# Kernel tuning notes

Hardware: AMD Instinct MI355X
Metric: run time of the kernel (lower is better)

The kernel has to match this reference:

```python
import jax, jax.numpy as jnp
import numpy as np

B, MAXN, NVT, NINP, NHID, NHEAD, NL, NZ = 1024, 32, 16, 256, 512, 8, 6, 64
HID = MAXN * NHID
EPS = 1e-5
SCALE = 1.0 / np.sqrt(NHID // NHEAD)


def setup_inputs() -> dict:
    key = jax.random.key(0)
    ks = jax.random.split(key, 16)
    s = 0.02
    d = {}
    d["node_types"] = jax.random.randint(ks[0], (B, MAXN), 0, NVT, dtype=jnp.int32)
    d["adj_bits"] = jax.random.randint(ks[1], (B, MAXN, MAXN), 0, 2, dtype=jnp.int32)
    d["Wpos"] = jax.random.normal(ks[2], (MAXN, NINP), jnp.float32) * s
    d["bpos"] = jnp.zeros((NINP,), jnp.float32)
    d["Wnode"] = jax.random.normal(ks[3], (NVT, NINP), jnp.float32) * s
    d["bnode"] = jnp.zeros((NINP,), jnp.float32)
    for i, n in enumerate(["Wq", "Wk", "Wv", "Wo", "W1", "W2"]):
        d["enc_" + n] = jax.random.normal(ks[4 + i], (NL, NHID, NHID), jnp.float32) * s
    for n in ["bq", "bk", "bv", "bo", "b1", "b2"]:
        d["enc_" + n] = jnp.zeros((NL, NHID), jnp.float32)
    d["ln1_g"] = jnp.ones((NL, NHID), jnp.float32)
    d["ln1_b"] = jnp.zeros((NL, NHID), jnp.float32)
    d["ln2_g"] = jnp.ones((NL, NHID), jnp.float32)
    d["ln2_b"] = jnp.zeros((NL, NHID), jnp.float32)
    d["Wfc1"] = jax.random.normal(ks[10], (HID, NZ), jnp.float32) * s
    d["bfc1"] = jnp.zeros((NZ,), jnp.float32)
    d["Wfc2"] = jax.random.normal(ks[11], (HID, NZ), jnp.float32) * s
    d["bfc2"] = jnp.zeros((NZ,), jnp.float32)
    return d


def _ln(x, g, b):
    m = x.mean(-1, keepdims=True)
    v = ((x - m) ** 2).mean(-1, keepdims=True)
    return (x - m) * jax.lax.rsqrt(v + EPS) * g + b


def _dag_attn_bias(adj_bits):
    # _mask_generate: transitive closure via matmul powers; log-depth squaring
    # over a boolean semiring (min(.,1) after each add) gives identical reachability.
    iu = jnp.triu(jnp.ones((MAXN, MAXN), jnp.float32), 1)  # enforce DAG
    adj = adj_bits.astype(jnp.float32) * iu  # [B,N,N]
    reach = adj
    for _ in range(int(np.ceil(np.log2(MAXN)))):
        reach = jnp.minimum(reach + jnp.matmul(reach, reach), 1.0)
    # original: mask = (sum_powers + I) < 0.5 (True=disallowed), then transpose(1,2)
    allowed = (jnp.swapaxes(reach, 1, 2) + jnp.eye(MAXN, dtype=jnp.float32)) > 0.5
    return jnp.where(allowed, 0.0, -jnp.inf)[:, None, :, :]  # [B,1,N,N]


def _encode(node_types, adj_bits, Wpos, bpos, Wnode, bnode,
            enc_Wq, enc_bq, enc_Wk, enc_bk, enc_Wv, enc_bv, enc_Wo, enc_bo,
            ln1_g, ln1_b, enc_W1, enc_b1, enc_W2, enc_b2, ln2_g, ln2_b,
            Wfc1, bfc1, Wfc2, bfc2):
    node_feat = jax.nn.relu(Wnode[node_types] + bnode)               # [B,N,ninp]
    pos_feat = jnp.broadcast_to(Wpos + bpos, (B, MAXN, NINP))        # position = node index
    x = jnp.concatenate([node_feat, pos_feat], -1)                   # [B,N,512]
    bias = _dag_attn_bias(adj_bits)
    dh = NHID // NHEAD
    for l in range(NL):
        q = (x @ enc_Wq[l] + enc_bq[l]).reshape(B, MAXN, NHEAD, dh)
        k = (x @ enc_Wk[l] + enc_bk[l]).reshape(B, MAXN, NHEAD, dh)
        v = (x @ enc_Wv[l] + enc_bv[l]).reshape(B, MAXN, NHEAD, dh)
        s = jnp.einsum('bqhd,bkhd->bhqk', q, k) * SCALE + bias
        a = jax.nn.softmax(s, axis=-1)
        o = jnp.einsum('bhqk,bkhd->bqhd', a, v).reshape(B, MAXN, NHID)
        x = _ln(x + o @ enc_Wo[l] + enc_bo[l], ln1_g[l], ln1_b[l])    # post-LN
        f = jax.nn.relu(x @ enc_W1[l] + enc_b1[l]) @ enc_W2[l] + enc_b2[l]
        x = _ln(x + f, ln2_g[l], ln2_b[l])
    mem = x.reshape(B, HID)
    return mem @ Wfc1 + bfc1, mem @ Wfc2 + bfc2


def reference(node_types, adj_bits, Wpos, bpos, Wnode, bnode,
              enc_Wq, enc_bq, enc_Wk, enc_bk, enc_Wv, enc_bv, enc_Wo, enc_bo,
              ln1_g, ln1_b, enc_W1, enc_b1, enc_W2, enc_b2, ln2_g, ln2_b,
              Wfc1, bfc1, Wfc2, bfc2):
    return _encode(node_types, adj_bits, Wpos, bpos, Wnode, bnode,
                   enc_Wq, enc_bq, enc_Wk, enc_bk, enc_Wv, enc_bv, enc_Wo, enc_bo,
                   ln1_g, ln1_b, enc_W1, enc_b1, enc_W2, enc_b2, ln2_g, ln2_b,
                   Wfc1, bfc1, Wfc2, bfc2)
```

## Files before the change

### kernel.cpp

```cpp
#include <hip/hip_runtime.h>


typedef unsigned short u16;
typedef unsigned int u32;
typedef __attribute__((ext_vector_type(8))) short bf16x8;
typedef __attribute__((ext_vector_type(4))) float f32x4;

#define NB 1024
#define MAXN 32
#define NHID 512
#define NHEAD 8
#define NLAY 6
#define MTOT (NB * MAXN)
#define ATT_SCALE 0.125f
#define LN_EPS 1e-5f

__device__ __forceinline__ float bf2f(u16 h) { return __uint_as_float(((u32)h) << 16); }
__device__ __forceinline__ u16 f2bf(float f) {
  u32 u = __float_as_uint(f);
  return (u16)((u + 0x7fffu + ((u >> 16) & 1u)) >> 16);
}

__device__ __forceinline__ void gload16(const void* g, void* l) {
  __builtin_amdgcn_global_load_lds((const __attribute__((address_space(1))) void*)g,
                                   (__attribute__((address_space(3))) void*)l, 16, 0, 0);
}

__global__ __launch_bounds__(256) void mask_k(const int* __restrict__ adj, u32* __restrict__ mask) {
  __shared__ u32 r[8][32];
  int tid = threadIdx.x;
  int g = tid >> 5, i = tid & 31;
  int b = blockIdx.x * 8 + g;
  const int* ab = adj + ((long)b * 32 + i) * 32;
  u32 m = 0;
  for (int j = i + 1; j < 32; ++j)
    if (ab[j]) m |= (1u << j);
  r[g][i] = m;
  __syncthreads();
  for (int it = 0; it < 5; ++it) {
    u32 cur = r[g][i];
    u32 acc = cur;
    #pragma unroll
    for (int j = 0; j < 32; ++j)
      if ((cur >> j) & 1u) acc |= r[g][j];
    __syncthreads();
    r[g][i] = acc;
    __syncthreads();
  }
  u32 am = 1u << i;
  #pragma unroll
  for (int k = 0; k < 32; ++k) am |= ((r[g][k] >> i) & 1u) << k;
  mask[b * 32 + i] = am;
}

__global__ __launch_bounds__(256) void embed_k(const int* __restrict__ types,
    const float* __restrict__ Wpos, const float* __restrict__ bpos,
    const float* __restrict__ Wnode, const float* __restrict__ bnode,
    float* __restrict__ x, u16* __restrict__ xb) {
  int i = blockIdx.x * 256 + threadIdx.x;
  int row = i >> 7, c = (i & 127) * 4;
  int b = row >> 5, n = row & 31;
  float v[4];
  if (c < 256) {
    int tp = types[b * 32 + n];
    const float* w = &Wnode[tp * 256 + c];
    #pragma unroll
    for (int j = 0; j < 4; ++j) v[j] = fmaxf(w[j] + bnode[c + j], 0.f);
  } else {
    int cc = c - 256;
    const float* w = &Wpos[n * 256 + cc];
    #pragma unroll
    for (int j = 0; j < 4; ++j) v[j] = w[j] + bpos[cc + j];
  }
  long o = (long)row * NHID + c;
  *(float4*)&x[o] = make_float4(v[0], v[1], v[2], v[3]);
  ushort4 h; h.x = f2bf(v[0]); h.y = f2bf(v[1]); h.z = f2bf(v[2]); h.w = f2bf(v[3]);
  *(ushort4*)&xb[o] = h;
}

__global__ __launch_bounds__(256) void tconv_k(const float* __restrict__ W,
    u16* __restrict__ Wt, int n_off, int n_total) {
  __shared__ float tile[32][33];
  int l = blockIdx.z;
  int k0 = blockIdx.x * 32, n0 = blockIdx.y * 32;
  int tx = threadIdx.x & 31, ty = threadIdx.x >> 5;
  const float* src = W + (size_t)l * NHID * NHID;
  #pragma unroll
  for (int i = 0; i < 4; ++i)
    tile[ty + 8 * i][tx] = src[(size_t)(k0 + ty + 8 * i) * NHID + n0 + tx];
  __syncthreads();
  u16* dst = Wt + (size_t)l * n_total * NHID;
  #pragma unroll
  for (int i = 0; i < 4; ++i)
    dst[(size_t)(n_off + n0 + ty + 8 * i) * NHID + k0 + tx] = f2bf(tile[tx][ty + 8 * i]);
}

template <int EPI>
__global__ __launch_bounds__(256, 2) void gemm_bt(
    const u16* __restrict__ A, const u16* __restrict__ Bt,
    const float* __restrict__ bias0, const float* __restrict__ bias1,
    const float* __restrict__ bias2, u16* __restrict__ Cout, int N, int K) {
  __shared__ u16 As[128 * 32];
  __shared__ u16 Bs[128 * 32];
  const int tid = threadIdx.x;
  const int wave = tid >> 6, lane = tid & 63;
  const long m0 = (long)blockIdx.y * 128;
  const int n0 = blockIdx.x * 128;
  const int wr = wave >> 1, wc = wave & 1;
  const int srow = lane >> 2;
  const int skof = (lane & 3) * 8;
  const int fr = lane & 15;
  const int kq = lane >> 4;
  f32x4 acc[4][4] = {};

  for (int k0 = 0; k0 < K; k0 += 32) {
    #pragma unroll
    for (int i = 0; i < 2; ++i) {
      int c = 2 * wave + i;
      gload16(A + (m0 + 16 * c + srow) * (long)K + k0 + skof, &As[c * 512]);
      gload16(Bt + (long)(n0 + 16 * c + srow) * K + k0 + skof, &Bs[c * 512]);
    }
    __syncthreads();
    bf16x8 af[4], bfr[4];
    #pragma unroll
    for (int mi = 0; mi < 4; ++mi)
      af[mi] = *(const bf16x8*)&As[(wr * 64 + mi * 16 + fr) * 32 + kq * 8];
    #pragma unroll
    for (int ni = 0; ni < 4; ++ni)
      bfr[ni] = *(const bf16x8*)&Bs[(wc * 64 + ni * 16 + fr) * 32 + kq * 8];
    #pragma unroll
    for (int mi = 0; mi < 4; ++mi)
      #pragma unroll
      for (int ni = 0; ni < 4; ++ni)
        acc[mi][ni] = __builtin_amdgcn_mfma_f32_16x16x32_bf16(af[mi], bfr[ni], acc[mi][ni], 0, 0, 0);
    __syncthreads();
  }

  #pragma unroll
  for (int ni = 0; ni < 4; ++ni) {
    int n = n0 + wc * 64 + ni * 16 + fr;
    const float* bp = (n < 512) ? bias0 : ((n < 1024) ? bias1 : bias2);
    float bias = bp[n & 511];
    #pragma unroll
    for (int mi = 0; mi < 4; ++mi) {
      long r = m0 + wr * 64 + mi * 16 + kq * 4;
      #pragma unroll
      for (int j = 0; j < 4; ++j) {
        float v = acc[mi][ni][j] + bias;
        if (EPI == 2) v = fmaxf(v, 0.f);
        Cout[(r + j) * (long)N + n] = f2bf(v);
      }
    }
  }
}

__global__ __launch_bounds__(256) void attn_k(const u16* __restrict__ qkv,
    const u32* __restrict__ mask, u16* __restrict__ o) {
  __shared__ u16 p_lds[4][32][40];
  int tid = threadIdx.x;
  int w = tid >> 6, lane = tid & 63;
  int idx = blockIdx.x * 4 + w;
  int b = idx >> 3, h = idx & 7;
  const u16* base = qkv + (long)b * 32 * 1536;
  int g = lane >> 4, r = lane & 15;

  f32x4 s[2][2] = {};
  #pragma unroll
  for (int ks = 0; ks < 2; ++ks) {
    bf16x8 kf[2], qf[2];
    #pragma unroll
    for (int mi = 0; mi < 2; ++mi)
      kf[mi] = *(const bf16x8*)(base + (long)(mi * 16 + r) * 1536 + 512 + h * 64 + ks * 32 + g * 8);
    #pragma unroll
    for (int nj = 0; nj < 2; ++nj)
      qf[nj] = *(const bf16x8*)(base + (long)(nj * 16 + r) * 1536 + h * 64 + ks * 32 + g * 8);
    #pragma unroll
    for (int mi = 0; mi < 2; ++mi)
      #pragma unroll
      for (int nj = 0; nj < 2; ++nj)
        s[mi][nj] = __builtin_amdgcn_mfma_f32_16x16x32_bf16(kf[mi], qf[nj], s[mi][nj], 0, 0, 0);
  }

  #pragma unroll
  for (int nj = 0; nj < 2; ++nj) {
    int q = nj * 16 + r;
    u32 mk = mask[b * 32 + q];
    float v[8];
    float mx = -1e30f;
    #pragma unroll
    for (int mi = 0; mi < 2; ++mi)
      #pragma unroll
      for (int j = 0; j < 4; ++j) {
        int k = mi * 16 + g * 4 + j;
        float val = ((mk >> k) & 1u) ? s[mi][nj][j] * ATT_SCALE : -1e30f;
        v[mi * 4 + j] = val;
        mx = fmaxf(mx, val);
      }
    mx = fmaxf(mx, __shfl_xor(mx, 16));
    mx = fmaxf(mx, __shfl_xor(mx, 32));
    float sum = 0.f;
    #pragma unroll
    for (int i = 0; i < 8; ++i) { v[i] = __expf(v[i] - mx); sum += v[i]; }
    sum += __shfl_xor(sum, 16);
    sum += __shfl_xor(sum, 32);
    float inv = 1.f / sum;
    #pragma unroll
    for (int mi = 0; mi < 2; ++mi) {
      ushort4 pk;
      pk.x = f2bf(v[mi * 4 + 0] * inv);
      pk.y = f2bf(v[mi * 4 + 1] * inv);
      pk.z = f2bf(v[mi * 4 + 2] * inv);
      pk.w = f2bf(v[mi * 4 + 3] * inv);
      *(ushort4*)&p_lds[w][q][mi * 16 + g * 4] = pk;
    }
  }
  __syncthreads();

  bf16x8 pa[2];
  #pragma unroll
  for (int mi = 0; mi < 2; ++mi)
    pa[mi] = *(const bf16x8*)&p_lds[w][mi * 16 + r][g * 8];
  f32x4 oacc[2][4] = {};
  #pragma unroll
  for (int nd = 0; nd < 4; ++nd) {
    bf16x8 vf;
    #pragma unroll
    for (int t = 0; t < 8; ++t)
      vf[t] = *(const short*)(base + (long)(g * 8 + t) * 1536 + 1024 + h * 64 + nd * 16 + r);
    #pragma unroll
    for (int mi = 0; mi < 2; ++mi)
      oacc[mi][nd] = __builtin_amdgcn_mfma_f32_16x16x32_bf16(pa[mi], vf, oacc[mi][nd], 0, 0, 0);
  }
  #pragma unroll
  for (int mi = 0; mi < 2; ++mi)
    #pragma unroll
    for (int j = 0; j < 4; ++j) {
      int q = mi * 16 + g * 4 + j;
      u16* og = o + ((long)b * 32 + q) * NHID + h * 64;
      #pragma unroll
      for (int nd = 0; nd < 4; ++nd)
        og[nd * 16 + r] = f2bf(oacc[mi][nd][j]);
    }
}

__global__ __launch_bounds__(256) void ln_k(float* xio, const u16* __restrict__ t,
    const float* __restrict__ g, const float* __restrict__ b, u16* __restrict__ xb) {
  __shared__ float ps[4], psq[4];
  int tid = threadIdx.x;
  int half = tid >> 7, lt = tid & 127;
  long row = (long)blockIdx.x * 2 + half;
  int c = lt * 4;
  long o = row * NHID + c;
  float4 xv = *(const float4*)&xio[o];
  ushort4 tv = *(const ushort4*)&t[o];
  float y[4] = {xv.x + bf2f(tv.x), xv.y + bf2f(tv.y), xv.z + bf2f(tv.z), xv.w + bf2f(tv.w)};
  float s = y[0] + y[1] + y[2] + y[3];
  float sq = y[0] * y[0] + y[1] * y[1] + y[2] * y[2] + y[3] * y[3];
  #pragma unroll
  for (int off = 32; off; off >>= 1) {
    s += __shfl_down(s, off);
    sq += __shfl_down(sq, off);
  }
  int wave = tid >> 6;
  if ((tid & 63) == 0) { ps[wave] = s; psq[wave] = sq; }
  __syncthreads();
  int w0 = half * 2;
  float S = ps[w0] + ps[w0 + 1], SQ = psq[w0] + psq[w0 + 1];
  float mean = S * (1.f / 512.f);
  float var = SQ * (1.f / 512.f) - mean * mean;
  float inv = rsqrtf(var + LN_EPS);
  float out[4];
  #pragma unroll
  for (int j = 0; j < 4; ++j) out[j] = (y[j] - mean) * inv * g[c + j] + b[c + j];
  *(float4*)&xio[o] = make_float4(out[0], out[1], out[2], out[3]);
  ushort4 hv; hv.x = f2bf(out[0]); hv.y = f2bf(out[1]); hv.z = f2bf(out[2]); hv.w = f2bf(out[3]);
  *(ushort4*)&xb[o] = hv;
}

__global__ __launch_bounds__(256) void fcT_k(const float* __restrict__ W1,
    const float* __restrict__ W2, u16* __restrict__ Wt) {
  __shared__ float t[64][65];
  int sel = blockIdx.y;
  const float* W = sel ? W2 : W1;
  int k0 = blockIdx.x * 64;
  int tx = threadIdx.x & 63, ty = threadIdx.x >> 6;
  #pragma unroll
  for (int i = 0; i < 16; ++i)
    t[ty + 4 * i][tx] = W[(long)(k0 + ty + 4 * i) * 64 + tx];
  __syncthreads();
  #pragma unroll
  for (int i = 0; i < 16; ++i)
    Wt[(long)(sel * 64 + ty + 4 * i) * 16384 + k0 + tx] = f2bf(t[tx][ty + 4 * i]);
}

__global__ __launch_bounds__(256, 2) void gemm_fc(const u16* __restrict__ A,
    const u16* __restrict__ Bt, float* __restrict__ part) {
  __shared__ u16 As[128 * 32];
  __shared__ u16 Bs[128 * 32];
  const int tid = threadIdx.x;
  const int wave = tid >> 6, lane = tid & 63;
  const int ks = blockIdx.x;
  const long m0 = (long)blockIdx.y * 128;
  const int kbase = ks * 512;
  const int wr = wave >> 1, wc = wave & 1;
  const int srow = lane >> 2;
  const int skof = (lane & 3) * 8;
  const int fr = lane & 15;
  const int kq = lane >> 4;
  f32x4 acc[4][4] = {};
  for (int k0 = 0; k0 < 512; k0 += 32) {
    #pragma unroll
    for (int i = 0; i < 2; ++i) {
      int c = 2 * wave + i;
      gload16(A + (m0 + 16 * c + srow) * 16384L + kbase + k0 + skof, &As[c * 512]);
      gload16(Bt + (long)(16 * c + srow) * 16384L + kbase + k0 + skof, &Bs[c * 512]);
    }
    __syncthreads();
    bf16x8 af[4], bfr[4];
    #pragma unroll
    for (int mi = 0; mi < 4; ++mi)
      af[mi] = *(const bf16x8*)&As[(wr * 64 + mi * 16 + fr) * 32 + kq * 8];
    #pragma unroll
    for (int ni = 0; ni < 4; ++ni)
      bfr[ni] = *(const bf16x8*)&Bs[(wc * 64 + ni * 16 + fr) * 32 + kq * 8];
    #pragma unroll
    for (int mi = 0; mi < 4; ++mi)
      #pragma unroll
      for (int ni = 0; ni < 4; ++ni)
        acc[mi][ni] = __builtin_amdgcn_mfma_f32_16x16x32_bf16(af[mi], bfr[ni], acc[mi][ni], 0, 0, 0);
    __syncthreads();
  }
  #pragma unroll
  for (int ni = 0; ni < 4; ++ni) {
    int n = wc * 64 + ni * 16 + fr;
    #pragma unroll
    for (int mi = 0; mi < 4; ++mi) {
      long rr = m0 + wr * 64 + mi * 16 + kq * 4;
      #pragma unroll
      for (int j = 0; j < 4; ++j)
        part[((long)ks * 1024 + rr + j) * 128 + n] = acc[mi][ni][j];
    }
  }
}

__global__ __launch_bounds__(256) void fc_red_k(const float* __restrict__ part,
    const float* __restrict__ bfc1, const float* __restrict__ bfc2,
    float* __restrict__ out) {
  int idx = blockIdx.x * 256 + threadIdx.x;
  int sel = idx >> 16;
  int rem = idx & 65535;
  int b = rem >> 6, z = rem & 63;
  float v = sel ? bfc2[z] : bfc1[z];
  #pragma unroll
  for (int ks = 0; ks < 32; ++ks)
    v += part[((long)ks * 1024 + b) * 128 + sel * 64 + z];
  out[idx] = v;
}

extern "C" void kernel_launch(void* const* d_in, const int* in_sizes, int n_in,
                              void* d_out, int out_size, void* d_ws, size_t ws_size,
                              hipStream_t stream) {
  const int* node_types = (const int*)d_in[0];
  const int* adj_bits = (const int*)d_in[1];
  const float* Wpos = (const float*)d_in[2];
  const float* bpos = (const float*)d_in[3];
  const float* Wnode = (const float*)d_in[4];
  const float* bnode = (const float*)d_in[5];
  const float* eWq = (const float*)d_in[6];
  const float* eWk = (const float*)d_in[7];
  const float* eWv = (const float*)d_in[8];
  const float* eWo = (const float*)d_in[9];
  const float* eW1 = (const float*)d_in[10];
  const float* eW2 = (const float*)d_in[11];
  const float* ebq = (const float*)d_in[12];
  const float* ebk = (const float*)d_in[13];
  const float* ebv = (const float*)d_in[14];
  const float* ebo = (const float*)d_in[15];
  const float* eb1 = (const float*)d_in[16];
  const float* eb2 = (const float*)d_in[17];
  const float* ln1g = (const float*)d_in[18];
  const float* ln1b = (const float*)d_in[19];
  const float* ln2g = (const float*)d_in[20];
  const float* ln2b = (const float*)d_in[21];
  const float* Wfc1 = (const float*)d_in[22];
  const float* bfc1 = (const float*)d_in[23];
  const float* Wfc2 = (const float*)d_in[24];
  const float* bfc2 = (const float*)d_in[25];

  char* ws = (char*)d_ws;
  size_t off = 0;
  auto carve = [&](size_t bytes) {
    void* p = ws + off;
    off += (bytes + 255) & ~(size_t)255;
    return p;
  };
  u16* Wqkv_t = (u16*)carve((size_t)NLAY * 1536 * 512 * 2);
  u16* Wo_t = (u16*)carve((size_t)NLAY * 512 * 512 * 2);
  u16* W1_t = (u16*)carve((size_t)NLAY * 512 * 512 * 2);
  u16* W2_t = (u16*)carve((size_t)NLAY * 512 * 512 * 2);
  float* xf = (float*)carve((size_t)MTOT * NHID * 4);
  u16* xb = (u16*)carve((size_t)MTOT * NHID * 2);
  u16* qkv = (u16*)carve((size_t)MTOT * 1536 * 2);
  u16* obuf = (u16*)carve((size_t)MTOT * NHID * 2);
  u32* maskb = (u32*)carve((size_t)NB * MAXN * 4);
  u16* tmp16 = qkv;
  u16* hbuf = obuf;
  u16* Wt_fc = qkv;
  float* part_fc = (float*)obuf;

  mask_k<<<NB / 8, 256, 0, stream>>>(adj_bits, maskb);
  embed_k<<<(MTOT * 128) / 256, 256, 0, stream>>>(node_types, Wpos, bpos, Wnode, bnode, xf, xb);
  dim3 tg(16, 16, NLAY);
  tconv_k<<<tg, 256, 0, stream>>>(eWq, Wqkv_t, 0, 1536);
  tconv_k<<<tg, 256, 0, stream>>>(eWk, Wqkv_t, 512, 1536);
  tconv_k<<<tg, 256, 0, stream>>>(eWv, Wqkv_t, 1024, 1536);
  tconv_k<<<tg, 256, 0, stream>>>(eWo, Wo_t, 0, 512);
  tconv_k<<<tg, 256, 0, stream>>>(eW1, W1_t, 0, 512);
  tconv_k<<<tg, 256, 0, stream>>>(eW2, W2_t, 0, 512);

  for (int l = 0; l < NLAY; ++l) {
    size_t lw = (size_t)l * 512 * 512;
    gemm_bt<1><<<dim3(12, MTOT / 128), 256, 0, stream>>>(
        xb, Wqkv_t + (size_t)l * 1536 * 512,
        ebq + l * 512, ebk + l * 512, ebv + l * 512, qkv, 1536, 512);
    attn_k<<<NB * NHEAD / 4, 256, 0, stream>>>(qkv, maskb, obuf);
    gemm_bt<1><<<dim3(4, MTOT / 128), 256, 0, stream>>>(
        obuf, Wo_t + lw, ebo + l * 512, ebo + l * 512, ebo + l * 512, tmp16, 512, 512);
    ln_k<<<MTOT / 2, 256, 0, stream>>>(xf, tmp16, ln1g + l * 512, ln1b + l * 512, xb);
    gemm_bt<2><<<dim3(4, MTOT / 128), 256, 0, stream>>>(
        xb, W1_t + lw, eb1 + l * 512, eb1 + l * 512, eb1 + l * 512, hbuf, 512, 512);
    gemm_bt<1><<<dim3(4, MTOT / 128), 256, 0, stream>>>(
        hbuf, W2_t + lw, eb2 + l * 512, eb2 + l * 512, eb2 + l * 512, tmp16, 512, 512);
    ln_k<<<MTOT / 2, 256, 0, stream>>>(xf, tmp16, ln2g + l * 512, ln2b + l * 512, xb);
  }

  fcT_k<<<dim3(256, 2), 256, 0, stream>>>(Wfc1, Wfc2, Wt_fc);
  gemm_fc<<<dim3(32, 8), 256, 0, stream>>>(xb, Wt_fc, part_fc);
  fc_red_k<<<512, 256, 0, stream>>>(part_fc, bfc1, bfc2, (float*)d_out);
}
```

Before: 1.567 ms.

## Fuse residual LayerNorm into full-row GEMM; double-buffer and swizzle GEMM LDS tiles

Adds a gemm_ln kernel in which each block computes 64 full 512-wide output rows. The epilogue applies bias, adds the residual, reduces row statistics through shuffles and LDS, and writes LayerNorm results in fp32 and bf16. This removes the separate ln_k launches and the bf16 round trip through a temporary buffer. All GEMMs also get double-buffered LDS staging so the next tile loads during compute, plus an XOR swizzle to cut LDS bank conflicts. The trade-off is fewer blocks for the fused GEMM (512), more LDS and registers per block, and lower occupancy.

```diff
diff --git a/kernel.cpp b/kernel.cpp
--- a/kernel.cpp
+++ b/kernel.cpp
@@ -100,39 +100,48 @@
     const u16* __restrict__ A, const u16* __restrict__ Bt,
     const float* __restrict__ bias0, const float* __restrict__ bias1,
     const float* __restrict__ bias2, u16* __restrict__ Cout, int N, int K) {
-  __shared__ u16 As[128 * 32];
-  __shared__ u16 Bs[128 * 32];
+  __shared__ u16 AsB[2][128 * 32];
+  __shared__ u16 BsB[2][128 * 32];
   const int tid = threadIdx.x;
   const int wave = tid >> 6, lane = tid & 63;
   const long m0 = (long)blockIdx.y * 128;
   const int n0 = blockIdx.x * 128;
   const int wr = wave >> 1, wc = wave & 1;
   const int srow = lane >> 2;
-  const int skof = (lane & 3) * 8;
+  const int sg = (lane & 3) ^ (srow & 3);
   const int fr = lane & 15;
   const int kq = lane >> 4;
   f32x4 acc[4][4] = {};
 
-  for (int k0 = 0; k0 < K; k0 += 32) {
+  auto stage = [&](int buf, int k0) {
     #pragma unroll
     for (int i = 0; i < 2; ++i) {
       int c = 2 * wave + i;
-      gload16(A + (m0 + 16 * c + srow) * (long)K + k0 + skof, &As[c * 512]);
-      gload16(Bt + (long)(n0 + 16 * c + srow) * K + k0 + skof, &Bs[c * 512]);
-    }
-    __syncthreads();
-    bf16x8 af[4], bfr[4];
-    #pragma unroll
-    for (int mi = 0; mi < 4; ++mi)
-      af[mi] = *(const bf16x8*)&As[(wr * 64 + mi * 16 + fr) * 32 + kq * 8];
+      gload16(A + (m0 + 16 * c + srow) * (long)K + k0 + sg * 8, &AsB[buf][c * 512]);
+      gload16(Bt + (long)(n0 + 16 * c + srow) * K + k0 + sg * 8, &BsB[buf][c * 512]);
+    }
+  };
+  stage(0, 0);
+  __syncthreads();
+  const int nt = K >> 5;
+  const int kqx = (kq ^ (fr & 3)) * 8;
+  for (int t = 0; t < nt; ++t) {
+    int cur = t & 1;
+    if (t + 1 < nt) stage(cur ^ 1, (t + 1) * 32);
+    const u16* As = AsB[cur];
+    const u16* Bs = BsB[cur];
+    bf16x8 af[4], bfv[4];
+    #pragma unroll
+    for (int mi = 0; mi < 4; ++mi)
+      af[mi] = *(const bf16x8*)&As[(wr * 64 + mi * 16 + fr) * 32 + kqx];
     #pragma unroll
     for (int ni = 0; ni < 4; ++ni)
-      bfr[ni] = *(const bf16x8*)&Bs[(wc * 64 + ni * 16 + fr) * 32 + kq * 8];
+      bfv[ni] = *(const bf16x8*)&Bs[(wc * 64 + ni * 16 + fr) * 32 + kqx];
     #pragma unroll
     for (int mi = 0; mi < 4; ++mi)
       #pragma unroll
       for (int ni = 0; ni < 4; ++ni)
-        acc[mi][ni] = __builtin_amdgcn_mfma_f32_16x16x32_bf16(af[mi], bfr[ni], acc[mi][ni], 0, 0, 0);
+        acc[mi][ni] = __builtin_amdgcn_mfma_f32_16x16x32_bf16(af[mi], bfv[ni], acc[mi][ni], 0, 0, 0);
     __syncthreads();
   }
 
@@ -152,6 +161,115 @@
       }
     }
   }
+}
+
+__global__ __launch_bounds__(256, 2) void gemm_ln(
+    const u16* __restrict__ A, const u16* __restrict__ Bt,
+    const float* __restrict__ bias, const float* __restrict__ g,
+    const float* __restrict__ b, float* __restrict__ xf, u16* __restrict__ xb) {
+  __shared__ u16 AsB[2][64 * 32];
+  __shared__ u16 BsB[2][512 * 32];
+  __shared__ float ps[4][64][2];
+  const int tid = threadIdx.x;
+  const int wave = tid >> 6, lane = tid & 63;
+  const long m0 = (long)blockIdx.x * 64;
+  const int srow = lane >> 2;
+  const int sg = (lane & 3) ^ (srow & 3);
+  const int fr = lane & 15;
+  const int kq = lane >> 4;
+  const int colbase = wave * 128;
+  f32x4 acc[4][8] = {};
+
+  auto stage = [&](int buf, int k0) {
+    gload16(A + (m0 + wave * 16 + srow) * 512L + k0 + sg * 8, &AsB[buf][wave * 512]);
+    #pragma unroll
+    for (int i = 0; i < 8; ++i) {
+      int c = wave * 8 + i;
+      gload16(Bt + (long)(c * 16 + srow) * 512 + k0 + sg * 8, &BsB[buf][c * 512]);
+    }
+  };
+  stage(0, 0);
+  __syncthreads();
+  const int kqx = (kq ^ (fr & 3)) * 8;
+  for (int t = 0; t < 16; ++t) {
+    int cur = t & 1;
+    if (t < 15) stage(cur ^ 1, (t + 1) * 32);
+    const u16* As = AsB[cur];
+    const u16* Bs = BsB[cur];
+    bf16x8 af[4], bfv[8];
+    #pragma unroll
+    for (int mi = 0; mi < 4; ++mi)
+      af[mi] = *(const bf16x8*)&As[(mi * 16 + fr) * 32 + kqx];
+    #pragma unroll
+    for (int ni = 0; ni < 8; ++ni)
+      bfv[ni] = *(const bf16x8*)&Bs[(colbase + ni * 16 + fr) * 32 + kqx];
+    #pragma unroll
+    for (int mi = 0; mi < 4; ++mi)
+      #pragma unroll
+      for (int ni = 0; ni < 8; ++ni)
+        acc[mi][ni] = __builtin_amdgcn_mfma_f32_16x16x32_bf16(af[mi], bfv[ni], acc[mi][ni], 0, 0, 0);
+    __syncthreads();
+  }
+
+  float bv[8], gv[8], bb[8];
+  #pragma unroll
+  for (int ni = 0; ni < 8; ++ni) {
+    int c = colbase + ni * 16 + fr;
+    bv[ni] = bias[c]; gv[ni] = g[c]; bb[ni] = b[c];
+  }
+  float s16[4][4], q16[4][4];
+  #pragma unroll
+  for (int mi = 0; mi < 4; ++mi)
+    #pragma unroll
+    for (int j = 0; j < 4; ++j) {
+      long row = m0 + mi * 16 + kq * 4 + j;
+      float s = 0.f, sq = 0.f;
+      #pragma unroll
+      for (int ni = 0; ni < 8; ++ni) {
+        float y = acc[mi][ni][j] + bv[ni] + xf[row * 512 + colbase + ni * 16 + fr];
+        acc[mi][ni][j] = y;
+        s += y; sq += y * y;
+      }
+      s16[mi][j] = s; q16[mi][j] = sq;
+    }
+  #pragma unroll
+  for (int off = 1; off < 16; off <<= 1)
+    #pragma unroll
+    for (int mi = 0; mi < 4; ++mi)
+      #pragma unroll
+      for (int j = 0; j < 4; ++j) {
+        s16[mi][j] += __shfl_xor(s16[mi][j], off);
+        q16[mi][j] += __shfl_xor(q16[mi][j], off);
+      }
+  if (fr == 0) {
+    #pragma unroll
+    for (int mi = 0; mi < 4; ++mi)
+      #pragma unroll
+      for (int j = 0; j < 4; ++j) {
+        int r = mi * 16 + kq * 4 + j;
+        ps[wave][r][0] = s16[mi][j];
+        ps[wave][r][1] = q16[mi][j];
+      }
+  }
+  __syncthreads();
+  #pragma unroll
+  for (int mi = 0; mi < 4; ++mi)
+    #pragma unroll
+    for (int j = 0; j < 4; ++j) {
+      int r = mi * 16 + kq * 4 + j;
+      float S = ps[0][r][0] + ps[1][r][0] + ps[2][r][0] + ps[3][r][0];
+      float Q = ps[0][r][1] + ps[1][r][1] + ps[2][r][1] + ps[3][r][1];
+      float mean = S * (1.f / 512.f);
+      float inv = rsqrtf(Q * (1.f / 512.f) - mean * mean + LN_EPS);
+      long row = m0 + r;
+      #pragma unroll
+      for (int ni = 0; ni < 8; ++ni) {
+        float o = (acc[mi][ni][j] - mean) * inv * gv[ni] + bb[ni];
+        long idx = row * 512 + colbase + ni * 16 + fr;
+        xf[idx] = o;
+        xb[idx] = f2bf(o);
+      }
+    }
 }
 
 __global__ __launch_bounds__(256) void attn_k(const u16* __restrict__ qkv,
@@ -243,40 +361,6 @@
     }
 }
 
-__global__ __launch_bounds__(256) void ln_k(float* xio, const u16* __restrict__ t,
-    const float* __restrict__ g, const float* __restrict__ b, u16* __restrict__ xb) {
-  __shared__ float ps[4], psq[4];
-  int tid = threadIdx.x;
-  int half = tid >> 7, lt = tid & 127;
-  long row = (long)blockIdx.x * 2 + half;
-  int c = lt * 4;
-  long o = row * NHID + c;
-  float4 xv = *(const float4*)&xio[o];
-  ushort4 tv = *(const ushort4*)&t[o];
-  float y[4] = {xv.x + bf2f(tv.x), xv.y + bf2f(tv.y), xv.z + bf2f(tv.z), xv.w + bf2f(tv.w)};
-  float s = y[0] + y[1] + y[2] + y[3];
-  float sq = y[0] * y[0] + y[1] * y[1] + y[2] * y[2] + y[3] * y[3];
-  #pragma unroll
-  for (int off = 32; off; off >>= 1) {
-    s += __shfl_down(s, off);
-    sq += __shfl_down(sq, off);
-  }
-  int wave = tid >> 6;
-  if ((tid & 63) == 0) { ps[wave] = s; psq[wave] = sq; }
-  __syncthreads();
-  int w0 = half * 2;
-  float S = ps[w0] + ps[w0 + 1], SQ = psq[w0] + psq[w0 + 1];
-  float mean = S * (1.f / 512.f);
-  float var = SQ * (1.f / 512.f) - mean * mean;
-  float inv = rsqrtf(var + LN_EPS);
-  float out[4];
-  #pragma unroll
-  for (int j = 0; j < 4; ++j) out[j] = (y[j] - mean) * inv * g[c + j] + b[c + j];
-  *(float4*)&xio[o] = make_float4(out[0], out[1], out[2], out[3]);
-  ushort4 hv; hv.x = f2bf(out[0]); hv.y = f2bf(out[1]); hv.z = f2bf(out[2]); hv.w = f2bf(out[3]);
-  *(ushort4*)&xb[o] = hv;
-}
-
 __global__ __launch_bounds__(256) void fcT_k(const float* __restrict__ W1,
     const float* __restrict__ W2, u16* __restrict__ Wt) {
   __shared__ float t[64][65];
@@ -295,8 +379,8 @@
 
 __global__ __launch_bounds__(256, 2) void gemm_fc(const u16* __restrict__ A,
     const u16* __restrict__ Bt, float* __restrict__ part) {
-  __shared__ u16 As[128 * 32];
-  __shared__ u16 Bs[128 * 32];
+  __shared__ u16 AsB[2][128 * 32];
+  __shared__ u16 BsB[2][128 * 32];
   const int tid = threadIdx.x;
   const int wave = tid >> 6, lane = tid & 63;
   const int ks = blockIdx.x;
@@ -304,30 +388,38 @@
   const int kbase = ks * 512;
   const int wr = wave >> 1, wc = wave & 1;
   const int srow = lane >> 2;
-  const int skof = (lane & 3) * 8;
+  const int sg = (lane & 3) ^ (srow & 3);
   const int fr = lane & 15;
   const int kq = lane >> 4;
   f32x4 acc[4][4] = {};
-  for (int k0 = 0; k0 < 512; k0 += 32) {
+  auto stage = [&](int buf, int k0) {
     #pragma unroll
     for (int i = 0; i < 2; ++i) {
       int c = 2 * wave + i;
-      gload16(A + (m0 + 16 * c + srow) * 16384L + kbase + k0 + skof, &As[c * 512]);
-      gload16(Bt + (long)(16 * c + srow) * 16384L + kbase + k0 + skof, &Bs[c * 512]);
-    }
-    __syncthreads();
-    bf16x8 af[4], bfr[4];
-    #pragma unroll
-    for (int mi = 0; mi < 4; ++mi)
-      af[mi] = *(const bf16x8*)&As[(wr * 64 + mi * 16 + fr) * 32 + kq * 8];
+      gload16(A + (m0 + 16 * c + srow) * 16384L + kbase + k0 + sg * 8, &AsB[buf][c * 512]);
+      gload16(Bt + (long)(16 * c + srow) * 16384L + kbase + k0 + sg * 8, &BsB[buf][c * 512]);
+    }
+  };
+  stage(0, 0);
+  __syncthreads();
+  const int kqx = (kq ^ (fr & 3)) * 8;
+  for (int t = 0; t < 16; ++t) {
+    int cur = t & 1;
+    if (t < 15) stage(cur ^ 1, (t + 1) * 32);
+    const u16* As = AsB[cur];
+    const u16* Bs = BsB[cur];
+    bf16x8 af[4], bfv[4];
+    #pragma unroll
+    for (int mi = 0; mi < 4; ++mi)
+      af[mi] = *(const bf16x8*)&As[(wr * 64 + mi * 16 + fr) * 32 + kqx];
     #pragma unroll
     for (int ni = 0; ni < 4; ++ni)
-      bfr[ni] = *(const bf16x8*)&Bs[(wc * 64 + ni * 16 + fr) * 32 + kq * 8];
+      bfv[ni] = *(const bf16x8*)&Bs[(wc * 64 + ni * 16 + fr) * 32 + kqx];
     #pragma unroll
     for (int mi = 0; mi < 4; ++mi)
       #pragma unroll
       for (int ni = 0; ni < 4; ++ni)
-        acc[mi][ni] = __builtin_amdgcn_mfma_f32_16x16x32_bf16(af[mi], bfr[ni], acc[mi][ni], 0, 0, 0);
+        acc[mi][ni] = __builtin_amdgcn_mfma_f32_16x16x32_bf16(af[mi], bfv[ni], acc[mi][ni], 0, 0, 0);
     __syncthreads();
   }
   #pragma unroll
@@ -403,7 +495,6 @@
   u16* qkv = (u16*)carve((size_t)MTOT * 1536 * 2);
   u16* obuf = (u16*)carve((size_t)MTOT * NHID * 2);
   u32* maskb = (u32*)carve((size_t)NB * MAXN * 4);
-  u16* tmp16 = qkv;
   u16* hbuf = obuf;
   u16* Wt_fc = qkv;
   float* part_fc = (float*)obuf;
@@ -424,14 +515,12 @@
         xb, Wqkv_t + (size_t)l * 1536 * 512,
         ebq + l * 512, ebk + l * 512, ebv + l * 512, qkv, 1536, 512);
     attn_k<<<NB * NHEAD / 4, 256, 0, stream>>>(qkv, maskb, obuf);
-    gemm_bt<1><<<dim3(4, MTOT / 128), 256, 0, stream>>>(
-        obuf, Wo_t + lw, ebo + l * 512, ebo + l * 512, ebo + l * 512, tmp16, 512, 512);
-    ln_k<<<MTOT / 2, 256, 0, stream>>>(xf, tmp16, ln1g + l * 512, ln1b + l * 512, xb);
+    gemm_ln<<<MTOT / 64, 256, 0, stream>>>(
+        obuf, Wo_t + lw, ebo + l * 512, ln1g + l * 512, ln1b + l * 512, xf, xb);
     gemm_bt<2><<<dim3(4, MTOT / 128), 256, 0, stream>>>(
         xb, W1_t + lw, eb1 + l * 512, eb1 + l * 512, eb1 + l * 512, hbuf, 512, 512);
-    gemm_bt<1><<<dim3(4, MTOT / 128), 256, 0, stream>>>(
-        hbuf, W2_t + lw, eb2 + l * 512, eb2 + l * 512, eb2 + l * 512, tmp16, 512, 512);
-    ln_k<<<MTOT / 2, 256, 0, stream>>>(xf, tmp16, ln2g + l * 512, ln2b + l * 512, xb);
+    gemm_ln<<<MTOT / 64, 256, 0, stream>>>(
+        hbuf, W2_t + lw, eb2 + l * 512, ln2g + l * 512, ln2b + l * 512, xf, xb);
   }
 
   fcT_k<<<dim3(256, 2), 256, 0, stream>>>(Wfc1, Wfc2, Wt_fc);
```

Result: slower. 1.920 ms (+22.5%).
